# Kernel optimization log

Measured on AMD Instinct MI355X. Metric: run time of the kernel, lower is better.

Reference implementation:

```python
import jax, jax.numpy as jnp
import numpy as np

NUM_HEADS = 12
THETA = 10000.0


def _rope(x, pos):
    # x: [B, H, S, dk]; interleaved even/odd pair rotation
    dk = x.shape[-1]
    freqs = THETA ** (-jnp.arange(dk // 2, dtype=jnp.float32) * 2.0 / dk)  # [dk/2]
    ang = pos.astype(jnp.float32)[:, None] * freqs                         # [S, dk/2]
    cos, sin = jnp.cos(ang), jnp.sin(ang)
    x1, x2 = x[..., 0::2], x[..., 1::2]
    rot = jnp.stack([x1 * cos - x2 * sin, x1 * sin + x2 * cos], axis=-1)
    return rot.reshape(x.shape)


def setup_inputs() -> dict:
    key = jax.random.key(0)
    ks = jax.random.split(key, 5)
    B, S, D = 4, 2048, 768
    w_scale = 1.0 / np.sqrt(D).astype(np.float32)
    x = jax.random.normal(ks[0], (B, S, D), dtype=jnp.float32)
    Wq = jax.random.normal(ks[1], (D, D), dtype=jnp.float32) * w_scale
    Wk = jax.random.normal(ks[2], (D, D), dtype=jnp.float32) * w_scale
    Wv = jax.random.normal(ks[3], (D, D), dtype=jnp.float32) * w_scale
    Wo = jax.random.normal(ks[4], (D, D), dtype=jnp.float32) * w_scale
    token_positions = jnp.arange(S, dtype=jnp.int32)
    return {"x": x, "Wq": Wq, "Wk": Wk, "Wv": Wv, "Wo": Wo,
            "token_positions": token_positions}


def reference(x, Wq, Wk, Wv, Wo, token_positions):
    B, S, D = x.shape
    H = NUM_HEADS
    dk = D // H
    # bias-free linear layers: y = x @ W^T (torch Linear weight convention)
    q = (x @ Wq.T).reshape(B, S, H, dk).transpose(0, 2, 1, 3)  # [B,H,S,dk]
    k = (x @ Wk.T).reshape(B, S, H, dk).transpose(0, 2, 1, 3)
    v = (x @ Wv.T).reshape(B, S, H, dk).transpose(0, 2, 1, 3)
    q = _rope(q, token_positions)
    k = _rope(k, token_positions)
    scores = jnp.einsum('bhqd,bhkd->bhqk', q, k) / np.float32(np.sqrt(dk))
    causal = jnp.tril(jnp.ones((S, S), dtype=bool))
    scores = jnp.where(causal, scores, -jnp.inf)
    attn = jax.nn.softmax(scores, axis=-1)                      # [B,H,S,S]
    out = jnp.einsum('bhqk,bhkd->bhqd', attn, v)
    out = out.transpose(0, 2, 1, 3).reshape(B, S, D)
    return out @ Wo.T
```

## Files before the change

### kernel.cpp

```cpp
#include <hip/hip_runtime.h>
#include <cstdint>
#include <cstddef>

#define NTOK 8192
#define SLEN 2048
#define DM   768
#define NH   12
#define DKH  64

typedef __attribute__((ext_vector_type(8))) short bf16x8;
typedef __attribute__((ext_vector_type(4))) float f32x4;

__device__ __forceinline__ float b2f(unsigned short u) {
  return __uint_as_float(((unsigned)u) << 16);
}
__device__ __forceinline__ unsigned short f2b(float f) {
  unsigned u = __float_as_uint(f);
  u += 0x7fffu + ((u >> 16) & 1u);
  return (unsigned short)(u >> 16);
}
__device__ __forceinline__ unsigned cvtpk(float lo, float hi) {
  unsigned r;
  asm("v_cvt_pk_bf16_f32 %0, %1, %2" : "=v"(r) : "v"(lo), "v"(hi));
  return r;
}

__device__ __forceinline__ void gld16(const void* g, void* l) {
  __builtin_amdgcn_global_load_lds(
      (const __attribute__((address_space(1))) void*)g,
      (__attribute__((address_space(3))) void*)l, 16, 0, 0);
}

#define BAR_DRAIN() do {                                  \
    asm volatile("s_waitcnt vmcnt(0)" ::: "memory");      \
    __builtin_amdgcn_s_barrier();                         \
    __builtin_amdgcn_sched_barrier(0);                    \
  } while (0)
#define BAR_KEEP4() do {                                  \
    asm volatile("s_waitcnt vmcnt(4)" ::: "memory");      \
    __builtin_amdgcn_s_barrier();                         \
    __builtin_amdgcn_sched_barrier(0);                    \
  } while (0)

__global__ void cast_all_kernel(const float* __restrict__ x,
                                const float* __restrict__ w0,
                                const float* __restrict__ w1,
                                const float* __restrict__ w2,
                                const float* __restrict__ w3,
                                unsigned short* __restrict__ xb,
                                unsigned short* __restrict__ wb) {
  const int bid = blockIdx.x, tid = threadIdx.x;
  const float* src;
  unsigned short* dst;
  size_t i;
  if (bid < 3072) {
    src = x; dst = xb; i = (size_t)bid * 256 + tid;
  } else {
    const int wbid = bid - 3072;
    const int w = wbid / 288;
    src = (w == 0) ? w0 : (w == 1) ? w1 : (w == 2) ? w2 : w3;
    dst = wb + (size_t)w * DM * DM;
    i = (size_t)(wbid - w * 288) * 256 + tid;
  }
  const float4* p = (const float4*)(src + i * 8);
  float4 a = p[0], b = p[1];
  union { unsigned short h[8]; bf16x8 v; } u;
  u.h[0] = f2b(a.x); u.h[1] = f2b(a.y); u.h[2] = f2b(a.z); u.h[3] = f2b(a.w);
  u.h[4] = f2b(b.x); u.h[5] = f2b(b.y); u.h[6] = f2b(b.z); u.h[7] = f2b(b.w);
  *(bf16x8*)(dst + i * 8) = u.v;
}

template <typename CT>
__global__ __launch_bounds__(256, 2) void gemm64_kernel(
    const unsigned short* __restrict__ A,
    const unsigned short* __restrict__ B0, const unsigned short* __restrict__ B1,
    const unsigned short* __restrict__ B2,
    CT* __restrict__ C0, CT* __restrict__ C1, CT* __restrict__ C2,
    unsigned short* __restrict__ VTout,
    int N, int K, const int* __restrict__ pos, int qkv_mode) {
  const unsigned short* Bp = (blockIdx.z == 0) ? B0 : (blockIdx.z == 1) ? B1 : B2;
  CT* Cp = (blockIdx.z == 0) ? C0 : (blockIdx.z == 1) ? C1 : C2;
  const int tid = threadIdx.x, wid = tid >> 6, lane = tid & 63;
  const int lrow = lane & 15, g = lane >> 4, lk8 = g * 8;
  const int m0 = blockIdx.y * 64, n0 = blockIdx.x * 128;
  const int wm = (wid >> 1) * 32, wn = (wid & 1) * 64;
  const int sr = wid * 8 + (lane >> 3), sc = (lane & 7) * 8;
  const int ssw = sc ^ ((sr & 7) << 3);
  __shared__ unsigned short At[64 * 64];
  __shared__ unsigned short Bt[128 * 64];
  f32x4 acc[2][4] = {};

  const unsigned short* ap = A  + (size_t)(m0 + sr) * K + ssw;
  const unsigned short* bp = Bp + (size_t)(n0 + sr) * K + ssw;

  int aoff[2][2], boff[2][4];
#pragma unroll
  for (int ks = 0; ks < 2; ++ks) {
#pragma unroll
    for (int mi = 0; mi < 2; ++mi) {
      int ra = wm + mi * 16 + lrow;
      aoff[ks][mi] = (ra * 64 + ((ks * 32 + lk8) ^ ((ra & 7) << 3))) * 2;
    }
#pragma unroll
    for (int ni = 0; ni < 4; ++ni) {
      int rb = wn + ni * 16 + lrow;
      boff[ks][ni] = (rb * 64 + ((ks * 32 + lk8) ^ ((rb & 7) << 3))) * 2;
    }
  }
  const char* Atc = (const char*)At;
  const char* Btc = (const char*)Bt;

  const int nk = K >> 6;
  for (int kk = 0; kk < nk; ++kk) {
    __syncthreads();
    gld16(ap,          &At[(wid * 8) * 64]);
    gld16(ap + 32 * K, &At[(32 + wid * 8) * 64]);
#pragma unroll
    for (int rnd = 0; rnd < 4; ++rnd)
      gld16(bp + rnd * 32 * K, &Bt[(rnd * 32 + wid * 8) * 64]);
    ap += 64; bp += 64;
    __syncthreads();
    bf16x8 af[2][2], bfr[2][4];
#pragma unroll
    for (int ks = 0; ks < 2; ++ks) {
#pragma unroll
      for (int mi = 0; mi < 2; ++mi)
        af[ks][mi] = *(const bf16x8*)(Atc + aoff[ks][mi]);
#pragma unroll
      for (int ni = 0; ni < 4; ++ni)
        bfr[ks][ni] = *(const bf16x8*)(Btc + boff[ks][ni]);
    }
#pragma unroll
    for (int ks = 0; ks < 2; ++ks)
#pragma unroll
      for (int mi = 0; mi < 2; ++mi)
#pragma unroll
        for (int ni = 0; ni < 4; ++ni)
          acc[mi][ni] = __builtin_amdgcn_mfma_f32_16x16x32_bf16(
              bfr[ks][ni], af[ks][mi], acc[mi][ni], 0, 0, 0);
  }

  if (qkv_mode && blockIdx.z == 2) {
#pragma unroll
    for (int mi = 0; mi < 2; ++mi) {
      const int m = m0 + wm + mi * 16 + lrow;
      const int bb = m >> 11, st = m & (SLEN - 1);
      const int scol = (st & ~63) | (st & 35) |
                       (((st >> 4) & 1) << 2) | (((st >> 2) & 1) << 3) |
                       (((st >> 3) & 1) << 4);
#pragma unroll
      for (int ni = 0; ni < 4; ++ni) {
        const int nb = n0 + wn + ni * 16 + g * 4;
        const int hh = nb >> 6, dd = nb & 63;
        unsigned short* dst =
            VTout + ((size_t)(bb * NH + hh) * DKH + dd) * SLEN + scol;
#pragma unroll
        for (int r = 0; r < 4; ++r)
          dst[(size_t)r * SLEN] = f2b(acc[mi][ni][r]);
      }
    }
    return;
  }

  if (qkv_mode) {
    float frq[4][2];
#pragma unroll
    for (int ni = 0; ni < 4; ++ni)
#pragma unroll
      for (int rp = 0; rp < 2; ++rp)
        frq[ni][rp] = exp2f(
            (float)(((wn + ni * 16 + g * 4 + rp * 2) & 63) >> 1) *
            -0.4152410118609203f);
#pragma unroll
    for (int mi = 0; mi < 2; ++mi) {
      const int m = m0 + wm + mi * 16 + lrow;
      const float ps = (float)pos[m & (SLEN - 1)];
#pragma unroll
      for (int ni = 0; ni < 4; ++ni)
#pragma unroll
        for (int rp = 0; rp < 2; ++rp) {
          float sn, cs;
          __sincosf(ps * frq[ni][rp], &sn, &cs);
          float x1 = acc[mi][ni][2 * rp], x2 = acc[mi][ni][2 * rp + 1];
          acc[mi][ni][2 * rp]     = fmaf(x1, cs, -x2 * sn);
          acc[mi][ni][2 * rp + 1] = fmaf(x1, sn, x2 * cs);
        }
    }
  }

#pragma unroll
  for (int mi = 0; mi < 2; ++mi) {
    const int m = m0 + wm + mi * 16 + lrow;
#pragma unroll
    for (int ni = 0; ni < 4; ++ni) {
      const int nb = n0 + wn + ni * 16 + g * 4;
      if constexpr (sizeof(CT) == 2) {
        union { unsigned u[2]; ushort4 s; } o;
        o.u[0] = cvtpk(acc[mi][ni][0], acc[mi][ni][1]);
        o.u[1] = cvtpk(acc[mi][ni][2], acc[mi][ni][3]);
        *(ushort4*)&Cp[(size_t)m * N + nb] = o.s;
      } else {
        *(f32x4*)&Cp[(size_t)m * N + nb] = acc[mi][ni];
      }
    }
  }
}

__global__ __launch_bounds__(256, 2) void attn_kernel(
    const unsigned short* __restrict__ Q, const unsigned short* __restrict__ Kg,
    const unsigned short* __restrict__ VT, unsigned short* __restrict__ O) {
  const int bh = blockIdx.x;
  const int qt = 15 - (int)blockIdx.y;
  const int b = bh / NH, h = bh - b * NH;
  const size_t base = ((size_t)b * SLEN) * DM + h * DKH;
  const size_t vbase = (size_t)bh * DKH * SLEN;
  const int tid = threadIdx.x, wid = tid >> 6, lane = tid & 63;
  const int lrow = lane & 15, g = lane >> 4;

  __shared__ unsigned short Kt[3][64 * 64];
  __shared__ unsigned short Vt[3][64 * 64];

  bf16x8 qf[2][2];
#pragma unroll
  for (int mi = 0; mi < 2; ++mi)
#pragma unroll
    for (int ks = 0; ks < 2; ++ks) {
      const int qrow = qt * 128 + wid * 32 + mi * 16 + lrow;
      union { unsigned short h[8]; bf16x8 v; } u;
      u.v = *(const bf16x8*)&Q[base + (size_t)qrow * DM + ks * 32 + g * 8];
#pragma unroll
      for (int j = 0; j < 8; ++j)
        u.h[j] = f2b(b2f(u.h[j]) * 0.18033688011112042f);
      qf[mi][ks] = u.v;
    }

  union { unsigned short h[8]; bf16x8 v; } one_u;
#pragma unroll
  for (int j = 0; j < 8; ++j) one_u.h[j] = 0x3F80;
  const bf16x8 ones = one_u.v;

  f32x4 oacc[2][4] = {};
  f32x4 l_acc[2] = {};
  const int qg0 = qt * 128 + wid * 32 + lrow;
  const int nkt = 2 * qt + 2;

  const int srow = wid * 8 + (lane >> 3);
  const int ssw = ((lane & 7) * 8) ^ ((srow & 7) << 3);
  const unsigned short* kp = Kg + base + (size_t)srow * DM + ssw;
  const unsigned short* vp = VT + vbase + (size_t)srow * SLEN + ssw;

  int roff[2][4];
#pragma unroll
  for (int ks = 0; ks < 2; ++ks)
#pragma unroll
    for (int ni = 0; ni < 4; ++ni) {
      int rr = ni * 16 + lrow;
      roff[ks][ni] = (rr * 64 + ((ks * 32 + g * 8) ^ ((rr & 7) << 3))) * 2;
    }

  auto stage = [&](int buf) {
    gld16(kp,            &Kt[buf][(wid * 8) * 64]);
    gld16(kp + 32 * DM,  &Kt[buf][(32 + wid * 8) * 64]);
    gld16(vp,            &Vt[buf][(wid * 8) * 64]);
    gld16(vp + 32 * SLEN, &Vt[buf][(32 + wid * 8) * 64]);
    kp += 64 * DM;
    vp += 64;
  };

  auto compute = [&](int kt, int buf) {
    const bool active = !(kt == 2 * qt + 1 && wid < 2);
    if (!active) return;
    const char* Ksb = (const char*)&Kt[buf][0];
    const char* Vsb = (const char*)&Vt[buf][0];

    f32x4 sa[2][4] = {};
    __builtin_amdgcn_s_setprio(1);
#pragma unroll
    for (int ks = 0; ks < 2; ++ks)
#pragma unroll
      for (int ni = 0; ni < 4; ++ni) {
        bf16x8 kf = *(const bf16x8*)(Ksb + roff[ks][ni]);
#pragma unroll
        for (int mi = 0; mi < 2; ++mi)
          sa[mi][ni] = __builtin_amdgcn_mfma_f32_16x16x32_bf16(
              kf, qf[mi][ks], sa[mi][ni], 0, 0, 0);
      }
    __builtin_amdgcn_s_setprio(0);

    const bool need_mask = (kt * 64 + 64 > qt * 128 + wid * 32);
    if (need_mask) {
      const int kb = kt * 64 + g * 4;
#pragma unroll
      for (int mi = 0; mi < 2; ++mi) {
        const int qg = qg0 + mi * 16;
#pragma unroll
        for (int ni = 0; ni < 4; ++ni)
#pragma unroll
          for (int r = 0; r < 4; ++r)
            if (kb + ni * 16 + r > qg) sa[mi][ni][r] = -1e30f;
      }
    }

#pragma unroll
    for (int mi = 0; mi < 2; ++mi)
#pragma unroll
      for (int ni = 0; ni < 4; ++ni)
#pragma unroll
        for (int r = 0; r < 4; ++r)
          sa[mi][ni][r] = exp2f(sa[mi][ni][r]);

    bf16x8 pf[2][2];
#pragma unroll
    for (int mi = 0; mi < 2; ++mi)
#pragma unroll
      for (int ks = 0; ks < 2; ++ks) {
        union { unsigned u[4]; bf16x8 v; } uu;
        uu.u[0] = cvtpk(sa[mi][2 * ks][0],     sa[mi][2 * ks][1]);
        uu.u[1] = cvtpk(sa[mi][2 * ks][2],     sa[mi][2 * ks][3]);
        uu.u[2] = cvtpk(sa[mi][2 * ks + 1][0], sa[mi][2 * ks + 1][1]);
        uu.u[3] = cvtpk(sa[mi][2 * ks + 1][2], sa[mi][2 * ks + 1][3]);
        pf[mi][ks] = uu.v;
      }

    __builtin_amdgcn_s_setprio(1);
#pragma unroll
    for (int ks = 0; ks < 2; ++ks) {
#pragma unroll
      for (int ni = 0; ni < 4; ++ni) {
        bf16x8 vf = *(const bf16x8*)(Vsb + roff[ks][ni]);
#pragma unroll
        for (int mi = 0; mi < 2; ++mi)
          oacc[mi][ni] = __builtin_amdgcn_mfma_f32_16x16x32_bf16(
              vf, pf[mi][ks], oacc[mi][ni], 0, 0, 0);
      }
#pragma unroll
      for (int mi = 0; mi < 2; ++mi)
        l_acc[mi] = __builtin_amdgcn_mfma_f32_16x16x32_bf16(
            ones, pf[mi][ks], l_acc[mi], 0, 0, 0);
    }
    __builtin_amdgcn_s_setprio(0);
  };

  stage(0);
  int buf = 0, bufn = 1;
  for (int kt = 0; kt < nkt; ++kt) {
    if (kt + 1 < nkt) {
      stage(bufn);
      BAR_KEEP4();
    } else {
      BAR_DRAIN();
    }
    compute(kt, buf);
    buf = bufn;
    bufn = (bufn == 2) ? 0 : bufn + 1;
  }

#pragma unroll
  for (int mi = 0; mi < 2; ++mi) {
    const float inv = 1.f / l_acc[mi][0];
    const int qrow = qt * 128 + wid * 32 + mi * 16 + lrow;
#pragma unroll
    for (int ni = 0; ni < 4; ++ni) {
      union { unsigned u[2]; ushort4 s; } o;
      o.u[0] = cvtpk(oacc[mi][ni][0] * inv, oacc[mi][ni][1] * inv);
      o.u[1] = cvtpk(oacc[mi][ni][2] * inv, oacc[mi][ni][3] * inv);
      *(ushort4*)&O[base + (size_t)qrow * DM + ni * 16 + g * 4] = o.s;
    }
  }
}

extern "C" void kernel_launch(void* const* d_in, const int* in_sizes, int n_in,
                              void* d_out, int out_size, void* d_ws, size_t ws_size,
                              hipStream_t stream) {
  const float* x  = (const float*)d_in[0];
  const float* Wq = (const float*)d_in[1];
  const float* Wk = (const float*)d_in[2];
  const float* Wv = (const float*)d_in[3];
  const float* Wo = (const float*)d_in[4];
  const int* pos  = (const int*)d_in[5];
  float* out = (float*)d_out;

  char* ws = (char*)d_ws;
  size_t off = 0;
  auto carve = [&](size_t bytes) -> void* {
    void* p = ws + off;
    off += (bytes + 255) & ~(size_t)255;
    return p;
  };
  unsigned short* xb  = (unsigned short*)carve((size_t)NTOK * DM * 2);
  unsigned short* wqb = (unsigned short*)carve((size_t)DM * DM * 2);
  unsigned short* wkb = (unsigned short*)carve((size_t)DM * DM * 2);
  unsigned short* wvb = (unsigned short*)carve((size_t)DM * DM * 2);
  unsigned short* wob = (unsigned short*)carve((size_t)DM * DM * 2);
  unsigned short* Qb  = (unsigned short*)carve((size_t)NTOK * DM * 2);
  unsigned short* Kb  = (unsigned short*)carve((size_t)NTOK * DM * 2);
  unsigned short* Ab  = (unsigned short*)carve((size_t)NTOK * DM * 2);
  unsigned short* VTb = (unsigned short*)carve((size_t)4 * NH * DKH * SLEN * 2);

  cast_all_kernel<<<dim3(3072 + 4 * 288), dim3(256), 0, stream>>>(
      x, Wq, Wk, Wv, Wo, xb, wqb);

  gemm64_kernel<unsigned short><<<dim3(6, 128, 3), dim3(256), 0, stream>>>(
      xb, wqb, wkb, wvb, Qb, Kb, Qb, VTb, DM, DM, pos, 1);

  attn_kernel<<<dim3(48, 16), dim3(256), 0, stream>>>(Qb, Kb, VTb, Ab);

  gemm64_kernel<float><<<dim3(6, 128, 1), dim3(256), 0, stream>>>(
      Ab, wob, wob, wob, out, out, out, nullptr, DM, DM, pos, 0);
}
```

Before: 126.7 us.

## Pair mirrored 64-row query tiles per attention block and raise occupancy

Each attention block now processes two 64-row query tiles, y and 31-y, over one shared K/V stream. Every block therefore does the same causal work, which removes the tail imbalance of the old one-128-row-tile-per-block scheme. The diagonal mask now applies only on each tile's own diagonal step, and launch bounds rise from 2 to 3 blocks per CU for both the GEMM and attention kernels. In exchange, K/V tiles are streamed more times in total, and the tighter register budget may cause spills.

```diff
diff --git a/kernel.cpp b/kernel.cpp
--- a/kernel.cpp
+++ b/kernel.cpp
@@ -71,7 +71,7 @@
 }
 
 template <typename CT>
-__global__ __launch_bounds__(256, 2) void gemm64_kernel(
+__global__ __launch_bounds__(256, 3) void gemm64_kernel(
     const unsigned short* __restrict__ A,
     const unsigned short* __restrict__ B0, const unsigned short* __restrict__ B1,
     const unsigned short* __restrict__ B2,
@@ -206,43 +206,46 @@
   }
 }
 
-__global__ __launch_bounds__(256, 2) void attn_kernel(
+__global__ __launch_bounds__(256, 3) void attn_kernel(
     const unsigned short* __restrict__ Q, const unsigned short* __restrict__ Kg,
     const unsigned short* __restrict__ VT, unsigned short* __restrict__ O) {
   const int bh = blockIdx.x;
-  const int qt = 15 - (int)blockIdx.y;
+  const int y = blockIdx.y;
+  const int qA = y, qB = 31 - y;
+  const int ntA = qA + 1, ntB = qB + 1;
   const int b = bh / NH, h = bh - b * NH;
   const size_t base = ((size_t)b * SLEN) * DM + h * DKH;
   const size_t vbase = (size_t)bh * DKH * SLEN;
   const int tid = threadIdx.x, wid = tid >> 6, lane = tid & 63;
   const int lrow = lane & 15, g = lane >> 4;
+  const int rloc = wid * 16 + lrow;
 
   __shared__ unsigned short Kt[3][64 * 64];
   __shared__ unsigned short Vt[3][64 * 64];
 
-  bf16x8 qf[2][2];
-#pragma unroll
-  for (int mi = 0; mi < 2; ++mi)
-#pragma unroll
-    for (int ks = 0; ks < 2; ++ks) {
-      const int qrow = qt * 128 + wid * 32 + mi * 16 + lrow;
-      union { unsigned short h[8]; bf16x8 v; } u;
-      u.v = *(const bf16x8*)&Q[base + (size_t)qrow * DM + ks * 32 + g * 8];
-#pragma unroll
-      for (int j = 0; j < 8; ++j)
-        u.h[j] = f2b(b2f(u.h[j]) * 0.18033688011112042f);
-      qf[mi][ks] = u.v;
-    }
+  bf16x8 qfA[2], qfB[2];
+#pragma unroll
+  for (int ks = 0; ks < 2; ++ks) {
+    union { unsigned short h[8]; bf16x8 v; } u;
+    u.v = *(const bf16x8*)&Q[base + (size_t)(qA * 64 + rloc) * DM + ks * 32 + g * 8];
+#pragma unroll
+    for (int j = 0; j < 8; ++j)
+      u.h[j] = f2b(b2f(u.h[j]) * 0.18033688011112042f);
+    qfA[ks] = u.v;
+    u.v = *(const bf16x8*)&Q[base + (size_t)(qB * 64 + rloc) * DM + ks * 32 + g * 8];
+#pragma unroll
+    for (int j = 0; j < 8; ++j)
+      u.h[j] = f2b(b2f(u.h[j]) * 0.18033688011112042f);
+    qfB[ks] = u.v;
+  }
 
   union { unsigned short h[8]; bf16x8 v; } one_u;
 #pragma unroll
   for (int j = 0; j < 8; ++j) one_u.h[j] = 0x3F80;
   const bf16x8 ones = one_u.v;
 
-  f32x4 oacc[2][4] = {};
-  f32x4 l_acc[2] = {};
-  const int qg0 = qt * 128 + wid * 32 + lrow;
-  const int nkt = 2 * qt + 2;
+  f32x4 oaccA[4] = {}, oaccB[4] = {};
+  f32x4 lA = {}, lB = {};
 
   const int srow = wid * 8 + (lane >> 3);
   const int ssw = ((lane & 7) * 8) ^ ((srow & 7) << 3);
@@ -259,68 +262,55 @@
     }
 
   auto stage = [&](int buf) {
-    gld16(kp,            &Kt[buf][(wid * 8) * 64]);
-    gld16(kp + 32 * DM,  &Kt[buf][(32 + wid * 8) * 64]);
-    gld16(vp,            &Vt[buf][(wid * 8) * 64]);
+    gld16(kp,             &Kt[buf][(wid * 8) * 64]);
+    gld16(kp + 32 * DM,   &Kt[buf][(32 + wid * 8) * 64]);
+    gld16(vp,             &Vt[buf][(wid * 8) * 64]);
     gld16(vp + 32 * SLEN, &Vt[buf][(32 + wid * 8) * 64]);
     kp += 64 * DM;
     vp += 64;
   };
 
-  auto compute = [&](int kt, int buf) {
-    const bool active = !(kt == 2 * qt + 1 && wid < 2);
-    if (!active) return;
+  auto computeSub = [&](const bf16x8 (&qf)[2], f32x4 (&oacc)[4], f32x4& l_acc,
+                        bool diag, int buf) {
     const char* Ksb = (const char*)&Kt[buf][0];
     const char* Vsb = (const char*)&Vt[buf][0];
 
-    f32x4 sa[2][4] = {};
+    f32x4 sa[4] = {};
     __builtin_amdgcn_s_setprio(1);
 #pragma unroll
     for (int ks = 0; ks < 2; ++ks)
 #pragma unroll
       for (int ni = 0; ni < 4; ++ni) {
         bf16x8 kf = *(const bf16x8*)(Ksb + roff[ks][ni]);
-#pragma unroll
-        for (int mi = 0; mi < 2; ++mi)
-          sa[mi][ni] = __builtin_amdgcn_mfma_f32_16x16x32_bf16(
-              kf, qf[mi][ks], sa[mi][ni], 0, 0, 0);
+        sa[ni] = __builtin_amdgcn_mfma_f32_16x16x32_bf16(
+            kf, qf[ks], sa[ni], 0, 0, 0);
       }
     __builtin_amdgcn_s_setprio(0);
 
-    const bool need_mask = (kt * 64 + 64 > qt * 128 + wid * 32);
-    if (need_mask) {
-      const int kb = kt * 64 + g * 4;
-#pragma unroll
-      for (int mi = 0; mi < 2; ++mi) {
-        const int qg = qg0 + mi * 16;
-#pragma unroll
-        for (int ni = 0; ni < 4; ++ni)
-#pragma unroll
-          for (int r = 0; r < 4; ++r)
-            if (kb + ni * 16 + r > qg) sa[mi][ni][r] = -1e30f;
-      }
-    }
-
-#pragma unroll
-    for (int mi = 0; mi < 2; ++mi)
+    if (diag) {
 #pragma unroll
       for (int ni = 0; ni < 4; ++ni)
 #pragma unroll
         for (int r = 0; r < 4; ++r)
-          sa[mi][ni][r] = exp2f(sa[mi][ni][r]);
-
-    bf16x8 pf[2][2];
-#pragma unroll
-    for (int mi = 0; mi < 2; ++mi)
-#pragma unroll
-      for (int ks = 0; ks < 2; ++ks) {
-        union { unsigned u[4]; bf16x8 v; } uu;
-        uu.u[0] = cvtpk(sa[mi][2 * ks][0],     sa[mi][2 * ks][1]);
-        uu.u[1] = cvtpk(sa[mi][2 * ks][2],     sa[mi][2 * ks][3]);
-        uu.u[2] = cvtpk(sa[mi][2 * ks + 1][0], sa[mi][2 * ks + 1][1]);
-        uu.u[3] = cvtpk(sa[mi][2 * ks + 1][2], sa[mi][2 * ks + 1][3]);
-        pf[mi][ks] = uu.v;
-      }
+          if (ni * 16 + g * 4 + r > rloc) sa[ni][r] = -1e30f;
+    }
+
+#pragma unroll
+    for (int ni = 0; ni < 4; ++ni)
+#pragma unroll
+      for (int r = 0; r < 4; ++r)
+        sa[ni][r] = exp2f(sa[ni][r]);
+
+    bf16x8 pf[2];
+#pragma unroll
+    for (int ks = 0; ks < 2; ++ks) {
+      union { unsigned u[4]; bf16x8 v; } uu;
+      uu.u[0] = cvtpk(sa[2 * ks][0],     sa[2 * ks][1]);
+      uu.u[1] = cvtpk(sa[2 * ks][2],     sa[2 * ks][3]);
+      uu.u[2] = cvtpk(sa[2 * ks + 1][0], sa[2 * ks + 1][1]);
+      uu.u[3] = cvtpk(sa[2 * ks + 1][2], sa[2 * ks + 1][3]);
+      pf[ks] = uu.v;
+    }
 
     __builtin_amdgcn_s_setprio(1);
 #pragma unroll
@@ -328,42 +318,49 @@
 #pragma unroll
       for (int ni = 0; ni < 4; ++ni) {
         bf16x8 vf = *(const bf16x8*)(Vsb + roff[ks][ni]);
-#pragma unroll
-        for (int mi = 0; mi < 2; ++mi)
-          oacc[mi][ni] = __builtin_amdgcn_mfma_f32_16x16x32_bf16(
-              vf, pf[mi][ks], oacc[mi][ni], 0, 0, 0);
+        oacc[ni] = __builtin_amdgcn_mfma_f32_16x16x32_bf16(
+            vf, pf[ks], oacc[ni], 0, 0, 0);
       }
-#pragma unroll
-      for (int mi = 0; mi < 2; ++mi)
-        l_acc[mi] = __builtin_amdgcn_mfma_f32_16x16x32_bf16(
-            ones, pf[mi][ks], l_acc[mi], 0, 0, 0);
+      l_acc = __builtin_amdgcn_mfma_f32_16x16x32_bf16(
+          ones, pf[ks], l_acc, 0, 0, 0);
     }
     __builtin_amdgcn_s_setprio(0);
   };
 
   stage(0);
   int buf = 0, bufn = 1;
-  for (int kt = 0; kt < nkt; ++kt) {
-    if (kt + 1 < nkt) {
+  for (int t = 0; t < ntB; ++t) {
+    if (t + 1 < ntB) {
       stage(bufn);
       BAR_KEEP4();
     } else {
       BAR_DRAIN();
     }
-    compute(kt, buf);
+    if (t < ntA) computeSub(qfA, oaccA, lA, t == qA, buf);
+    computeSub(qfB, oaccB, lB, t == qB, buf);
     buf = bufn;
     bufn = (bufn == 2) ? 0 : bufn + 1;
   }
 
-#pragma unroll
-  for (int mi = 0; mi < 2; ++mi) {
-    const float inv = 1.f / l_acc[mi][0];
-    const int qrow = qt * 128 + wid * 32 + mi * 16 + lrow;
+  {
+    const float inv = 1.f / lA[0];
+    const int qrow = qA * 64 + rloc;
 #pragma unroll
     for (int ni = 0; ni < 4; ++ni) {
       union { unsigned u[2]; ushort4 s; } o;
-      o.u[0] = cvtpk(oacc[mi][ni][0] * inv, oacc[mi][ni][1] * inv);
-      o.u[1] = cvtpk(oacc[mi][ni][2] * inv, oacc[mi][ni][3] * inv);
+      o.u[0] = cvtpk(oaccA[ni][0] * inv, oaccA[ni][1] * inv);
+      o.u[1] = cvtpk(oaccA[ni][2] * inv, oaccA[ni][3] * inv);
+      *(ushort4*)&O[base + (size_t)qrow * DM + ni * 16 + g * 4] = o.s;
+    }
+  }
+  {
+    const float inv = 1.f / lB[0];
+    const int qrow = qB * 64 + rloc;
+#pragma unroll
+    for (int ni = 0; ni < 4; ++ni) {
+      union { unsigned u[2]; ushort4 s; } o;
+      o.u[0] = cvtpk(oaccB[ni][0] * inv, oaccB[ni][1] * inv);
+      o.u[1] = cvtpk(oaccB[ni][2] * inv, oaccB[ni][3] * inv);
       *(ushort4*)&O[base + (size_t)qrow * DM + ni * 16 + g * 4] = o.s;
     }
   }
```

After: 125.2 us. Within noise of the previous version (-1.2%).
